# Kernel tuning notes

Hardware: AMD Instinct MI355X
Metric: run time of the kernel (lower is better)

Reference implementation:

```python
import jax, jax.numpy as jnp
import numpy as np
from jax.scipy.special import gammaln, xlogy

B, S, C = 2, 2048, 1536
H, DK, DV = 8, 64, 192
F_REL = C // H  # 192 relative-position features


def positional_features_all(positions, feature_size, seq_length):
    # positions: [1, 2S-1] float32 (signed relative distances)
    n = feature_size // 6  # basis per class per sign
    ap = jnp.abs(positions)  # [1, 2S-1]
    Sf = float(seq_length)
    # exponential decay features
    max_range = float(np.log(Sf) / np.log(2.0))
    half_life = 2.0 ** jnp.linspace(3.0, max_range, n)  # min_half_life = 3.0
    feat_exp = jnp.exp(-jnp.log(2.0) / half_life * ap[..., None])
    # central mask features
    center_widths = 2.0 ** jnp.arange(1, n + 1, dtype=jnp.float32) - 1.0
    feat_cm = (center_widths > ap[..., None]).astype(jnp.float32)
    # gamma pdf features
    stddev = Sf / (2.0 * n)
    start_mean = Sf / n
    mean = jnp.linspace(start_mean, Sf, n)
    conc = (mean / stddev) ** 2
    rate = mean / (stddev ** 2)
    xg = ap[..., None]
    log_unnorm = xlogy(conc - 1.0, xg) - rate * xg
    log_norm = gammaln(conc) - conc * jnp.log(rate)
    prob = jnp.exp(log_unnorm - log_norm) + 1e-8
    feat_g = prob / jnp.max(prob, axis=1, keepdims=True)
    emb = jnp.concatenate([feat_exp, feat_cm, feat_g], axis=-1)  # [1, 2S-1, 3n]
    emb = jnp.concatenate([emb, jnp.sign(positions)[..., None] * emb], axis=-1)
    return emb  # [1, 2S-1, feature_size]


def relative_shift(x):
    # x: [B, H, T, 2T-1] -> [B, H, T, T] (Transformer-XL shift trick)
    b, h, t, _ = x.shape
    x = jnp.pad(x, ((0, 0), (0, 0), (0, 0), (1, 0)))  # [B,H,T,2T]
    x = x.reshape(b, h, 2 * t, t)[:, :, 1:, :]          # [B,H,2T-1,T]
    x = x.reshape(b, h, t, 2 * t - 1)[:, :, :, :t]      # [B,H,T,T]
    return x


def setup_inputs() -> dict:
    key = jax.random.key(0)
    ks = jax.random.split(key, 8)
    inp = {
        "x": jax.random.normal(ks[0], (B, S, C), dtype=jnp.float32),
        "mask": jax.random.randint(ks[1], (B, S), 0, 2, dtype=jnp.int32),
        "Wq": jax.random.normal(ks[2], (C, H * DK), dtype=jnp.float32) * 0.02,
        "Wk": jax.random.normal(ks[3], (C, H * DK), dtype=jnp.float32) * 0.02,
        "Wv": jax.random.normal(ks[4], (C, H * DV), dtype=jnp.float32) * 0.02,
        "Wr": jax.random.normal(ks[5], (F_REL, H * DK), dtype=jnp.float32) * 0.02,
        "r_w_bias": jax.random.normal(ks[6], (1, H, 1, DK), dtype=jnp.float32) * 0.02,
        "Wo": jax.random.normal(ks[7], (H * DV, H * DV), dtype=jnp.float32) * 0.02,
        "bo": jnp.zeros((H * DV,), dtype=jnp.float32),
    }
    return inp


def reference(x, mask, Wq, Wk, Wv, Wr, r_w_bias, Wo, bo):
    b, s, c = x.shape
    # projections -> [B, H, S, d]
    q = (x @ Wq).reshape(b, s, H, DK).transpose(0, 2, 1, 3) * (DK ** -0.5)
    k = (x @ Wk).reshape(b, s, H, DK).transpose(0, 2, 1, 3)
    v = (x @ Wv).reshape(b, s, H, DV).transpose(0, 2, 1, 3)
    # relative positional encodings for distances -S+1 .. S-1
    dist = jnp.arange(-s + 1, s, dtype=jnp.float32)[None, :]  # [1, 2S-1]
    pe = positional_features_all(dist, F_REL, s)               # [1, 2S-1, F_REL]
    r_k = (pe[0] @ Wr).reshape(2 * s - 1, H, DK).transpose(1, 0, 2)  # [H, 2S-1, DK]
    # content + position logits
    content_logits = jnp.einsum('bhqd,bhkd->bhqk', q, k)                   # [B,H,S,S]
    rel_logits = jnp.einsum('bhqd,hkd->bhqk', q + r_w_bias, r_k)           # [B,H,S,2S-1]
    logits = content_logits + relative_shift(rel_logits)
    logits = jnp.where(mask[:, None, None, :] == 0, -1e9, logits)
    weights = jax.nn.softmax(logits, axis=-1)
    out = jnp.einsum('bhqk,bhkd->bhqd', weights, v)  # [B,H,S,DV]
    out = out.transpose(0, 2, 1, 3).reshape(b, s, H * DV)
    return out @ Wo + bo
```

## Files before the change

kernel.cpp:

```cpp
#include <hip/hip_runtime.h>
#include <math.h>

#define SEQ 2048
#define CDIM 1536
#define HN 8
#define DVC 192
#define BN 2
#define NPOS 4095
#define HDK 512
#define HDV 1536
#define PSTR 72

typedef __attribute__((ext_vector_type(8))) _Float16 hf8v;
typedef __attribute__((ext_vector_type(4))) _Float16 hf4v;
typedef __attribute__((ext_vector_type(4))) float f4v;

static __device__ __forceinline__ f4v mfma16(hf8v a, hf8v b, f4v c) {
  return __builtin_amdgcn_mfma_f32_16x16x32_f16(a, b, c, 0, 0, 0);
}
static __device__ __forceinline__ void gl2lds16(const void* g, void* l) {
  __builtin_amdgcn_global_load_lds((const __attribute__((address_space(1))) unsigned int*)g,
                                   (__attribute__((address_space(3))) unsigned int*)l,
                                   16, 0, 0);
}
static __device__ __forceinline__ float rowmax16(float x) {
  x = fmaxf(x, __int_as_float(__builtin_amdgcn_update_dpp(0, __float_as_int(x), 0x128, 0xf, 0xf, true)));
  x = fmaxf(x, __int_as_float(__builtin_amdgcn_update_dpp(0, __float_as_int(x), 0x124, 0xf, 0xf, true)));
  x = fmaxf(x, __int_as_float(__builtin_amdgcn_update_dpp(0, __float_as_int(x), 0x122, 0xf, 0xf, true)));
  x = fmaxf(x, __int_as_float(__builtin_amdgcn_update_dpp(0, __float_as_int(x), 0x121, 0xf, 0xf, true)));
  return x;
}

#define CAST_B 6144
#define TWQ_B  768
#define TWK_B  768
#define TWV_B  2304
#define TWO_B  2304
#define TWR_B  96
#define PREP_BLOCKS (CAST_B + TWQ_B + TWK_B + TWV_B + TWO_B + TWR_B)

__device__ __forceinline__ void twc_tile(const float* __restrict__ W, _Float16* __restrict__ WT,
                                         int K, int N, int tile, float (*tls)[33], int tid) {
  int ntn = N >> 5;
  int nt = tile % ntn, kt = tile / ntn;
  int k0 = kt * 32, n0 = nt * 32;
  int tx = tid & 31, ty = tid >> 5;
#pragma unroll
  for (int p = 0; p < 4; p++) tls[ty + p * 8][tx] = W[(size_t)(k0 + ty + p * 8) * N + n0 + tx];
  __syncthreads();
#pragma unroll
  for (int p = 0; p < 4; p++) {
    int n = ty + p * 8;
    WT[(size_t)(n0 + n) * K + k0 + tx] = (_Float16)tls[tx][n];
  }
}

__global__ __launch_bounds__(256) void prep_kernel(
    const float* __restrict__ x, const float* __restrict__ Wq, const float* __restrict__ Wk,
    const float* __restrict__ Wv, const float* __restrict__ Wo, const float* __restrict__ Wr,
    _Float16* __restrict__ xb, _Float16* __restrict__ WTqkv, _Float16* __restrict__ WoT,
    _Float16* __restrict__ WrT) {
  __shared__ float tls[32][33];
  int blk = blockIdx.x, tid = threadIdx.x;
  if (blk < CAST_B) {
    int i = (blk * 256 + tid) * 4;
    float4 v = *(const float4*)(x + i);
    _Float16 o[4] = {(_Float16)v.x, (_Float16)v.y, (_Float16)v.z, (_Float16)v.w};
    *(unsigned long long*)(xb + i) = *(const unsigned long long*)o;
  } else if (blk < CAST_B + TWQ_B) {
    twc_tile(Wq, WTqkv + 0 * (size_t)CDIM, CDIM, HDK, blk - CAST_B, tls, tid);
  } else if (blk < CAST_B + TWQ_B + TWK_B) {
    twc_tile(Wk, WTqkv + 512 * (size_t)CDIM, CDIM, HDK, blk - (CAST_B + TWQ_B), tls, tid);
  } else if (blk < CAST_B + TWQ_B + TWK_B + TWV_B) {
    twc_tile(Wv, WTqkv + 1024 * (size_t)CDIM, CDIM, HDV, blk - (CAST_B + TWQ_B + TWK_B), tls, tid);
  } else if (blk < CAST_B + TWQ_B + TWK_B + TWV_B + TWO_B) {
    twc_tile(Wo, WoT, CDIM, HDV, blk - (CAST_B + TWQ_B + TWK_B + TWV_B), tls, tid);
  } else {
    twc_tile(Wr, WrT, 192, HDK, blk - (CAST_B + TWQ_B + TWK_B + TWV_B + TWO_B), tls, tid);
  }
}

__global__ __launch_bounds__(256) void pe_kernel(_Float16* __restrict__ pe_h) {
  int idx = blockIdx.x * 256 + threadIdx.x;
  int pos = idx / 96, f = idx - pos * 96;
  float val = 0.0f, sval = 0.0f;
  if (pos < NPOS) {
    float ap = fabsf((float)(pos - (SEQ - 1)));
    int j = f & 31, cls = f >> 5;
    if (cls == 0) {
      float hl = exp2f(3.0f + 8.0f * (float)j / 31.0f);
      val = exp2f(-ap / hl);
    } else if (cls == 1) {
      float cw = exp2f((float)(j + 1)) - 1.0f;
      val = (cw > ap) ? 1.0f : 0.0f;
    } else {
      float conc = 4.0f * (float)((j + 1) * (j + 1));
      float rate = (float)(j + 1) / 16.0f;
      float log_norm = lgammaf(conc) - conc * logf(rate);
      float pv = expf((conc - 1.0f) * logf(ap) - rate * ap - log_norm) + 1e-8f;
      float mode = (conc - 1.0f) / rate;
      float a0 = fminf(floorf(mode), 2047.0f);
      float a1 = fminf(a0 + 1.0f, 2047.0f);
      float p0 = expf((conc - 1.0f) * logf(a0) - rate * a0 - log_norm) + 1e-8f;
      float p1 = expf((conc - 1.0f) * logf(a1) - rate * a1 - log_norm) + 1e-8f;
      val = pv / fmaxf(p0, p1);
    }
    float sgn = (pos > SEQ - 1) ? 1.0f : ((pos < SEQ - 1) ? -1.0f : 0.0f);
    sval = sgn * val;
  }
  pe_h[pos * 192 + f] = (_Float16)val;
  pe_h[pos * 192 + 96 + f] = (_Float16)sval;
}

template <int MODE>
__global__ __launch_bounds__(256, 3) void mfma_gemm(
    const _Float16* __restrict__ A, const _Float16* __restrict__ B,
    const float* __restrict__ bias, void* __restrict__ out0, void* __restrict__ out1,
    void* __restrict__ out2, int K, int ntx) {
  __shared__ __align__(16) _Float16 As[128 * 64];
  __shared__ __align__(16) _Float16 Bs[128 * 64];
  const int tid = threadIdx.x;
  const int lane = tid & 63, l15 = lane & 15, quad = lane >> 4;
  const int wv = tid >> 6;
  const int wm = (wv & 1) * 64, wn = (wv >> 1) * 64;
  const int lin = blockIdx.x;
  const int cpx = gridDim.x >> 3;
  const int sw = (lin & 7) * cpx + (lin >> 3);
  const int row0 = (sw / ntx) * 128, col0 = (sw % ntx) * 128;
  f4v acc[4][4];
#pragma unroll
  for (int i = 0; i < 4; i++)
#pragma unroll
    for (int j = 0; j < 4; j++) acc[i][j] = (f4v)0.0f;

  for (int k0 = 0; k0 < K; k0 += 64) {
    __syncthreads();
#pragma unroll
    for (int p = 0; p < 4; p++) {
      int idx = tid + p * 256;
      int rr = idx >> 3, sc = idx & 7;
      int gc = (sc ^ (rr & 7)) << 3;
      gl2lds16(A + (size_t)(row0 + rr) * K + k0 + gc, As + idx * 8);
      gl2lds16(B + (size_t)(col0 + rr) * K + k0 + gc, Bs + idx * 8);
    }
    __syncthreads();
#pragma unroll
    for (int kc = 0; kc < 2; kc++) {
      hf8v af[4], bfr[4];
#pragma unroll
      for (int t = 0; t < 4; t++) {
        int lrA = wm + t * 16 + l15;
        int lrB = wn + t * 16 + l15;
        af[t]  = *(const hf8v*)(As + lrA * 64 + ((((kc << 2) | quad) ^ (lrA & 7)) << 3));
        bfr[t] = *(const hf8v*)(Bs + lrB * 64 + ((((kc << 2) | quad) ^ (lrB & 7)) << 3));
      }
#pragma unroll
      for (int mt = 0; mt < 4; mt++)
#pragma unroll
        for (int nt = 0; nt < 4; nt++)
          acc[mt][nt] = mfma16(af[mt], bfr[nt], acc[mt][nt]);
    }
  }
#pragma unroll
  for (int mt = 0; mt < 4; mt++)
#pragma unroll
    for (int reg = 0; reg < 4; reg++) {
      int r = row0 + wm + mt * 16 + quad * 4 + reg;
      int bb = r >> 11, ss = r & (SEQ - 1);
#pragma unroll
      for (int nt = 0; nt < 4; nt++) {
        int c = col0 + wn + nt * 16 + l15;
        float vv = acc[mt][nt][reg];
        if (MODE == 0) {
          if (c < 512) {
            ((_Float16*)out0)[(size_t)r * HDK + c] = (_Float16)(vv * 0.125f);
          } else if (c < 1024) {
            int cc = c - 512, h = cc >> 6, d = cc & 63;
            ((_Float16*)out1)[(((size_t)bb * HN + h) * SEQ + ss) * 64 + d] = (_Float16)vv;
          } else {
            int cc = c - 1024, h = cc / DVC, e = cc - h * DVC;
            int jp = (ss & ~63) | ((ss & 15) << 2) | ((ss >> 4) & 3);
            ((_Float16*)out2)[(((size_t)bb * HN + h) * DVC + e) * SEQ + jp] = (_Float16)vv;
          }
        } else if (MODE == 1) {
          int h = c >> 6, d = c & 63;
          ((_Float16*)out0)[((size_t)h * 4096 + r) * 64 + d] = (_Float16)vv;
        } else {
          ((float*)out0)[(size_t)r * HDV + c] = vv + bias[c];
        }
      }
    }
}

template <bool SPLITKV>
__global__ __launch_bounds__(256, 2) void attn_mfma(
    const _Float16* __restrict__ qb, const _Float16* __restrict__ kb,
    const _Float16* __restrict__ vtb, const _Float16* __restrict__ rkb,
    const float* __restrict__ rwb, const int* __restrict__ mask,
    _Float16* __restrict__ attn_out, _Float16* __restrict__ Opart, float* __restrict__ ml) {
  __shared__ __align__(16) _Float16 Vts[192 * 64];
  __shared__ __align__(16) _Float16 RKs[192 * 64];
  __shared__ __align__(16) _Float16 Kts[64 * 64];
  __shared__ __align__(16) _Float16 Pbs[128 * PSTR];

  const int lin = blockIdx.x;
  const int chunk = SPLITKV ? 64 : 32;
  const int swz = (lin & 7) * chunk + (lin >> 3);
  const int bx = swz & 15;
  const int by = swz >> 4;
  const int i0 = bx * 128;
  const int bh = SPLITKV ? (by & 15) : by;
  const int half = SPLITKV ? (by >> 4) : 0;
  const int b = bh >> 3, h = bh & 7;
  const int tid = threadIdx.x;
  const int wv = tid >> 6, lane = tid & 63;
  const int l15 = lane & 15, quad = lane >> 4;

  hf8v qf[2][2], qbf[2][2];
#pragma unroll
  for (int s = 0; s < 2; s++) {
    int qrow = i0 + wv * 32 + s * 16 + l15;
    const _Float16* qp = qb + (size_t)(b * SEQ + qrow) * HDK + h * 64;
#pragma unroll
    for (int kc = 0; kc < 2; kc++) {
      hf8v qv = *(const hf8v*)(qp + kc * 32 + quad * 8);
      qf[s][kc] = qv;
      hf8v t;
#pragma unroll
      for (int j = 0; j < 8; j++)
        t[j] = (_Float16)((float)qv[j] + rwb[h * 64 + kc * 32 + quad * 8 + j]);
      qbf[s][kc] = t;
    }
  }

  f4v Of[2][12];
#pragma unroll
  for (int s = 0; s < 2; s++)
#pragma unroll
    for (int se = 0; se < 12; se++) Of[s][se] = (f4v)0.0f;
  float m_i[2][4] = {{-INFINITY, -INFINITY, -INFINITY, -INFINITY},
                     {-INFINITY, -INFINITY, -INFINITY, -INFINITY}};
  float l_i[2][4] = {{0.f, 0.f, 0.f, 0.f}, {0.f, 0.f, 0.f, 0.f}};

  const int j0beg = SPLITKV ? half * (SEQ / 2) : 0;
  const int j0end = SPLITKV ? j0beg + SEQ / 2 : SEQ;

  for (int j0 = j0beg; j0 < j0end; j0 += 64) {
    __syncthreads();
    int mraw[4];
#pragma unroll
    for (int st = 0; st < 4; st++) mraw[st] = mask[b * SEQ + j0 + st * 16 + l15];
    {
      const int U0 = j0 - i0 + 1920;
#pragma unroll
      for (int r = 0; r < 2; r++) {
        int idx = tid + r * 256, row = idx >> 3, sc = idx & 7;
        gl2lds16(kb + ((size_t)bh * SEQ + j0 + row) * 64 + ((sc ^ (row & 7)) << 3), Kts + idx * 8);
      }
#pragma unroll
      for (int r = 0; r < 6; r++) {
        int idx = tid + r * 256, row = idx >> 3, sc = idx & 7;
        gl2lds16(rkb + ((size_t)h * 4096 + U0 + row) * 64 + ((sc ^ (row & 7)) << 3), RKs + idx * 8);
      }
#pragma unroll
      for (int r = 0; r < 6; r++) {
        int idx = tid + r * 256, row = idx >> 3, sc = idx & 7;
        gl2lds16(vtb + ((size_t)bh * DVC + row) * SEQ + j0 + ((sc ^ (row & 7)) << 3), Vts + idx * 8);
      }
    }
    asm volatile("s_waitcnt vmcnt(6)" ::: "memory");
    __builtin_amdgcn_s_barrier();
    __builtin_amdgcn_sched_barrier(0);
    float mv[4];
#pragma unroll
    for (int st = 0; st < 4; st++) mv[st] = mraw[st] ? 0.f : -1e9f;

#pragma unroll
    for (int s = 0; s < 2; s++) {
      __builtin_amdgcn_s_setprio(1);
      f4v Sf[4];
#pragma unroll
      for (int st = 0; st < 4; st++) {
        Sf[st] = (f4v)0.0f;
#pragma unroll
        for (int kc = 0; kc < 2; kc++) {
          int row = st * 16 + l15;
          hf8v kf = *(const hf8v*)(Kts + row * 64 + ((((kc << 2) | quad) ^ (row & 7)) << 3));
          Sf[st] = mfma16(qf[s][kc], kf, Sf[st]);
        }
      }
      f4v Rf[5];
      const int tb = 112 - 32 * wv - 16 * s;
#pragma unroll
      for (int u = 0; u < 5; u++) {
        Rf[u] = (f4v)0.0f;
#pragma unroll
        for (int kc = 0; kc < 2; kc++) {
          int row = tb + u * 16 + l15;
          hf8v rf = *(const hf8v*)(RKs + row * 64 + ((((kc << 2) | quad) ^ (row & 7)) << 3));
          Rf[u] = mfma16(qbf[s][kc], rf, Rf[u]);
        }
      }
      __builtin_amdgcn_s_setprio(0);
#pragma unroll
      for (int reg = 0; reg < 4; reg++) {
        int delta = l15 - (quad << 2) - reg + 15;
        int srcl = (quad << 4) | (delta & 15);
        float sh0 = __shfl(Rf[0][reg], srcl, 64);
        float sh1 = __shfl(Rf[1][reg], srcl, 64);
        float sh2 = __shfl(Rf[2][reg], srcl, 64);
        float sh3 = __shfl(Rf[3][reg], srcl, 64);
        float sh4 = __shfl(Rf[4][reg], srcl, 64);
        bool hib = delta >= 16;
        Sf[0][reg] += (hib ? sh1 : sh0) + mv[0];
        Sf[1][reg] += (hib ? sh2 : sh1) + mv[1];
        Sf[2][reg] += (hib ? sh3 : sh2) + mv[2];
        Sf[3][reg] += (hib ? sh4 : sh3) + mv[3];
      }
#pragma unroll
      for (int reg = 0; reg < 4; reg++) {
        float t = fmaxf(fmaxf(Sf[0][reg], Sf[1][reg]), fmaxf(Sf[2][reg], Sf[3][reg]));
        t = rowmax16(t);
        if (__any(t - m_i[s][reg] > 8.0f)) {
          float mn = fmaxf(m_i[s][reg], t);
          float alpha = __expf(m_i[s][reg] - mn);
          m_i[s][reg] = mn;
          l_i[s][reg] *= alpha;
#pragma unroll
          for (int se = 0; se < 12; se++) Of[s][se][reg] *= alpha;
        }
        float mcur = m_i[s][reg];
        hf4v pv;
        float rs = 0.f;
#pragma unroll
        for (int st = 0; st < 4; st++) {
          float p = __expf(Sf[st][reg] - mcur);
          rs += p;
          pv[st] = (_Float16)p;
        }
        l_i[s][reg] += rs;
        *(hf4v*)(Pbs + (size_t)(wv * 32 + s * 16 + quad * 4 + reg) * PSTR + l15 * 4) = pv;
      }
    }

    hf8v pa[2][2];
#pragma unroll
    for (int s = 0; s < 2; s++)
#pragma unroll
      for (int kc = 0; kc < 2; kc++)
        pa[s][kc] = *(const hf8v*)(Pbs + (size_t)(wv * 32 + s * 16 + l15) * PSTR +
                                   kc * 32 + quad * 8);
    asm volatile("s_waitcnt vmcnt(0)" ::: "memory");
    __builtin_amdgcn_s_barrier();
    __builtin_amdgcn_sched_barrier(0);
    __builtin_amdgcn_s_setprio(1);
#pragma unroll
    for (int se = 0; se < 12; se++) {
#pragma unroll
      for (int kc = 0; kc < 2; kc++) {
        int row = se * 16 + l15;
        hf8v vf = *(const hf8v*)(Vts + row * 64 + ((((kc << 2) | quad) ^ (row & 7)) << 3));
        Of[0][se] = mfma16(pa[0][kc], vf, Of[0][se]);
        Of[1][se] = mfma16(pa[1][kc], vf, Of[1][se]);
      }
    }
    __builtin_amdgcn_s_setprio(0);
  }

#pragma unroll
  for (int s = 0; s < 2; s++)
#pragma unroll
    for (int reg = 0; reg < 4; reg++) {
      float ls = l_i[s][reg];
      ls += __shfl_xor(ls, 1);
      ls += __shfl_xor(ls, 2);
      ls += __shfl_xor(ls, 4);
      ls += __shfl_xor(ls, 8);
      int row = i0 + wv * 32 + s * 16 + quad * 4 + reg;
      int rg = b * SEQ + row;
      float inv = 1.0f / ls;
      if constexpr (SPLITKV) {
        _Float16* Op = Opart + ((size_t)(half * 4096 + rg)) * HDV + h * DVC;
#pragma unroll
        for (int se = 0; se < 12; se++) Op[se * 16 + l15] = (_Float16)(Of[s][se][reg] * inv);
        if (l15 == 0) {
          size_t mlb = (((size_t)half * 4096 + rg) * HN + h) * 2;
          ml[mlb] = m_i[s][reg];
          ml[mlb + 1] = ls;
        }
      } else {
        size_t base2 = (size_t)rg * HDV + h * DVC;
#pragma unroll
        for (int se = 0; se < 12; se++)
          attn_out[base2 + se * 16 + l15] = (_Float16)(Of[s][se][reg] * inv);
      }
    }
}

__global__ __launch_bounds__(256) void combine_kernel(const _Float16* __restrict__ Opart,
                                                      const float* __restrict__ ml,
                                                      _Float16* __restrict__ attn_out) {
  int i4 = blockIdx.x * 256 + threadIdx.x;
  int rg = i4 / 384, c4 = (i4 - rg * 384) * 4;
  int h = c4 / DVC;
  size_t mlb0 = ((size_t)rg * HN + h) * 2;
  size_t mlb1 = (((size_t)4096 + rg) * HN + h) * 2;
  float m0 = ml[mlb0], l0 = ml[mlb0 + 1];
  float m1 = ml[mlb1], l1 = ml[mlb1 + 1];
  float M = fmaxf(m0, m1);
  float w0 = l0 * __expf(m0 - M), w1 = l1 * __expf(m1 - M);
  float inv = 1.0f / (w0 + w1);
  w0 *= inv;
  w1 *= inv;
  hf4v O0 = *(const hf4v*)(Opart + (size_t)rg * HDV + c4);
  hf4v O1 = *(const hf4v*)(Opart + ((size_t)4096 + rg) * HDV + c4);
  hf4v o;
#pragma unroll
  for (int q = 0; q < 4; q++) o[q] = (_Float16)((float)O0[q] * w0 + (float)O1[q] * w1);
  *(hf4v*)(attn_out + (size_t)rg * HDV + c4) = o;
}

extern "C" void kernel_launch(void* const* d_in, const int* in_sizes, int n_in,
                              void* d_out, int out_size, void* d_ws, size_t ws_size,
                              hipStream_t stream) {
  const float* x    = (const float*)d_in[0];
  const int*   mask = (const int*)d_in[1];
  const float* Wq   = (const float*)d_in[2];
  const float* Wk   = (const float*)d_in[3];
  const float* Wv   = (const float*)d_in[4];
  const float* Wr   = (const float*)d_in[5];
  const float* rwb  = (const float*)d_in[6];
  const float* Wo   = (const float*)d_in[7];
  const float* bo   = (const float*)d_in[8];
  float* out = (float*)d_out;

  char* wsb = (char*)d_ws;
  size_t o = 0;
  auto al = [](size_t v) { return (v + 255) & ~(size_t)255; };
#define CARVE(ptr_t, name, bytes) ptr_t name = (ptr_t)(wsb + o); o = al(o + (bytes));
  CARVE(_Float16*, pe_h, (size_t)4096 * 192 * 2)
  CARVE(_Float16*, WrT, (size_t)HDK * 192 * 2)
  CARVE(_Float16*, xb, (size_t)BN * SEQ * CDIM * 2)
  CARVE(_Float16*, WTqkv, (size_t)2560 * CDIM * 2)
  CARVE(_Float16*, WoT, (size_t)HDV * CDIM * 2)
  CARVE(_Float16*, qb, (size_t)BN * SEQ * HDK * 2)
  CARVE(_Float16*, kb, (size_t)BN * SEQ * HDK * 2)
  CARVE(_Float16*, vtb, (size_t)BN * SEQ * HDV * 2)
  CARVE(_Float16*, rkb, (size_t)HN * 4096 * 64 * 2)
  _Float16* attnh = xb;
  CARVE(_Float16*, Opart, (size_t)2 * 4096 * HDV * 2)
  CARVE(float*, ml, (size_t)2 * 4096 * HN * 2 * 4)
  bool dosplit = (o <= ws_size);

  prep_kernel<<<PREP_BLOCKS, 256, 0, stream>>>(x, Wq, Wk, Wv, Wo, Wr, xb, WTqkv, WoT, WrT);
  pe_kernel<<<4096 * 96 / 256, 256, 0, stream>>>(pe_h);
  mfma_gemm<0><<<640, 256, 0, stream>>>(xb, WTqkv, nullptr, qb, kb, vtb, CDIM, 20);
  mfma_gemm<1><<<128, 256, 0, stream>>>(pe_h, WrT, nullptr, rkb, nullptr, nullptr, 192, 4);
  if (dosplit) {
    attn_mfma<true><<<512, 256, 0, stream>>>(qb, kb, vtb, rkb, rwb, mask,
                                             attnh, Opart, ml);
    combine_kernel<<<4096 * 384 / 256, 256, 0, stream>>>(Opart, ml, attnh);
  } else {
    attn_mfma<false><<<256, 256, 0, stream>>>(qb, kb, vtb, rkb, rwb, mask,
                                              attnh, nullptr, nullptr);
  }
  mfma_gemm<2><<<384, 256, 0, stream>>>(attnh, WoT, bo, out, nullptr, nullptr, CDIM, 12);
}
```

Baseline: 306.7 us.

## Fuse split-KV combine into output projection GEMM with fp32 partials

Removes the separate combine kernel: the attention kernel now writes unnormalized fp32 partial outputs and the output-projection GEMM merges the two KV halves (max/sum rescale) while loading its A tiles. This saves one launch and the fp16 intermediate write/read, but every column tile of the GEMM now re-reads both fp32 partials and recomputes the merge weights, greatly increasing A-side memory traffic. The A loads are also done through registers rather than direct-to-LDS copies.

```diff
diff --git a/kernel.cpp b/kernel.cpp
--- a/kernel.cpp
+++ b/kernel.cpp
@@ -192,12 +192,98 @@
     }
 }
 
+__global__ __launch_bounds__(256, 2) void mfma_gemm_fc(
+    const float* __restrict__ Opart, const float* __restrict__ ml,
+    const _Float16* __restrict__ B, const float* __restrict__ bias,
+    float* __restrict__ out, int ntx) {
+  __shared__ __align__(16) _Float16 As[128 * 64];
+  __shared__ __align__(16) _Float16 Bs[128 * 64];
+  const int K = CDIM;
+  const int tid = threadIdx.x;
+  const int lane = tid & 63, l15 = lane & 15, quad = lane >> 4;
+  const int wv = tid >> 6;
+  const int wm = (wv & 1) * 64, wn = (wv >> 1) * 64;
+  const int lin = blockIdx.x;
+  const int cpx = gridDim.x >> 3;
+  const int sw = (lin & 7) * cpx + (lin >> 3);
+  const int row0 = (sw / ntx) * 128, col0 = (sw % ntx) * 128;
+  f4v acc[4][4];
+#pragma unroll
+  for (int i = 0; i < 4; i++)
+#pragma unroll
+    for (int j = 0; j < 4; j++) acc[i][j] = (f4v)0.0f;
+
+  for (int k0 = 0; k0 < K; k0 += 64) {
+    __syncthreads();
+#pragma unroll
+    for (int p = 0; p < 4; p++) {
+      int idx = tid + p * 256;
+      int rr = idx >> 3, sc = idx & 7;
+      int gc = (sc ^ (rr & 7)) << 3;
+      gl2lds16(B + (size_t)(col0 + rr) * K + k0 + gc, Bs + idx * 8);
+    }
+#pragma unroll
+    for (int p = 0; p < 4; p++) {
+      int idx = tid + p * 256;
+      int rr = idx >> 3, sc = idx & 7;
+      int gc = (sc ^ (rr & 7)) << 3;
+      int rg = row0 + rr;
+      int k = k0 + gc;
+      int h = k / DVC;
+      float2 ml0 = *(const float2*)(ml + (((size_t)rg) * HN + h) * 2);
+      float2 ml1 = *(const float2*)(ml + (((size_t)4096 + rg) * HN + h) * 2);
+      float M = fmaxf(ml0.x, ml1.x);
+      float w0 = __expf(ml0.x - M), w1 = __expf(ml1.x - M);
+      float inv = 1.0f / (ml0.y * w0 + ml1.y * w1);
+      w0 *= inv;
+      w1 *= inv;
+      const float* p0 = Opart + (size_t)rg * HDV + k;
+      const float* p1 = Opart + ((size_t)4096 + rg) * HDV + k;
+      float4 a0 = *(const float4*)(p0), b0 = *(const float4*)(p0 + 4);
+      float4 a1 = *(const float4*)(p1), b1 = *(const float4*)(p1 + 4);
+      _Float16 o[8] = {(_Float16)(a0.x * w0 + a1.x * w1), (_Float16)(a0.y * w0 + a1.y * w1),
+                       (_Float16)(a0.z * w0 + a1.z * w1), (_Float16)(a0.w * w0 + a1.w * w1),
+                       (_Float16)(b0.x * w0 + b1.x * w1), (_Float16)(b0.y * w0 + b1.y * w1),
+                       (_Float16)(b0.z * w0 + b1.z * w1), (_Float16)(b0.w * w0 + b1.w * w1)};
+      *(hf8v*)(As + idx * 8) = *(const hf8v*)o;
+    }
+    __syncthreads();
+#pragma unroll
+    for (int kc = 0; kc < 2; kc++) {
+      hf8v af[4], bfr[4];
+#pragma unroll
+      for (int t = 0; t < 4; t++) {
+        int lrA = wm + t * 16 + l15;
+        int lrB = wn + t * 16 + l15;
+        af[t]  = *(const hf8v*)(As + lrA * 64 + ((((kc << 2) | quad) ^ (lrA & 7)) << 3));
+        bfr[t] = *(const hf8v*)(Bs + lrB * 64 + ((((kc << 2) | quad) ^ (lrB & 7)) << 3));
+      }
+#pragma unroll
+      for (int mt = 0; mt < 4; mt++)
+#pragma unroll
+        for (int nt = 0; nt < 4; nt++)
+          acc[mt][nt] = mfma16(af[mt], bfr[nt], acc[mt][nt]);
+    }
+  }
+#pragma unroll
+  for (int mt = 0; mt < 4; mt++)
+#pragma unroll
+    for (int reg = 0; reg < 4; reg++) {
+      int r = row0 + wm + mt * 16 + quad * 4 + reg;
+#pragma unroll
+      for (int nt = 0; nt < 4; nt++) {
+        int c = col0 + wn + nt * 16 + l15;
+        out[(size_t)r * HDV + c] = acc[mt][nt][reg] + bias[c];
+      }
+    }
+}
+
 template <bool SPLITKV>
 __global__ __launch_bounds__(256, 2) void attn_mfma(
     const _Float16* __restrict__ qb, const _Float16* __restrict__ kb,
     const _Float16* __restrict__ vtb, const _Float16* __restrict__ rkb,
     const float* __restrict__ rwb, const int* __restrict__ mask,
-    _Float16* __restrict__ attn_out, _Float16* __restrict__ Opart, float* __restrict__ ml) {
+    _Float16* __restrict__ attn_out, float* __restrict__ Opart, float* __restrict__ ml) {
   __shared__ __align__(16) _Float16 Vts[192 * 64];
   __shared__ __align__(16) _Float16 RKs[192 * 64];
   __shared__ __align__(16) _Float16 Kts[64 * 64];
@@ -378,46 +464,23 @@
       ls += __shfl_xor(ls, 8);
       int row = i0 + wv * 32 + s * 16 + quad * 4 + reg;
       int rg = b * SEQ + row;
-      float inv = 1.0f / ls;
       if constexpr (SPLITKV) {
-        _Float16* Op = Opart + ((size_t)(half * 4096 + rg)) * HDV + h * DVC;
-#pragma unroll
-        for (int se = 0; se < 12; se++) Op[se * 16 + l15] = (_Float16)(Of[s][se][reg] * inv);
+        float* Op = Opart + ((size_t)(half * 4096 + rg)) * HDV + h * DVC;
+#pragma unroll
+        for (int se = 0; se < 12; se++) Op[se * 16 + l15] = Of[s][se][reg];
         if (l15 == 0) {
           size_t mlb = (((size_t)half * 4096 + rg) * HN + h) * 2;
           ml[mlb] = m_i[s][reg];
           ml[mlb + 1] = ls;
         }
       } else {
+        float inv = 1.0f / ls;
         size_t base2 = (size_t)rg * HDV + h * DVC;
 #pragma unroll
         for (int se = 0; se < 12; se++)
           attn_out[base2 + se * 16 + l15] = (_Float16)(Of[s][se][reg] * inv);
       }
     }
-}
-
-__global__ __launch_bounds__(256) void combine_kernel(const _Float16* __restrict__ Opart,
-                                                      const float* __restrict__ ml,
-                                                      _Float16* __restrict__ attn_out) {
-  int i4 = blockIdx.x * 256 + threadIdx.x;
-  int rg = i4 / 384, c4 = (i4 - rg * 384) * 4;
-  int h = c4 / DVC;
-  size_t mlb0 = ((size_t)rg * HN + h) * 2;
-  size_t mlb1 = (((size_t)4096 + rg) * HN + h) * 2;
-  float m0 = ml[mlb0], l0 = ml[mlb0 + 1];
-  float m1 = ml[mlb1], l1 = ml[mlb1 + 1];
-  float M = fmaxf(m0, m1);
-  float w0 = l0 * __expf(m0 - M), w1 = l1 * __expf(m1 - M);
-  float inv = 1.0f / (w0 + w1);
-  w0 *= inv;
-  w1 *= inv;
-  hf4v O0 = *(const hf4v*)(Opart + (size_t)rg * HDV + c4);
-  hf4v O1 = *(const hf4v*)(Opart + ((size_t)4096 + rg) * HDV + c4);
-  hf4v o;
-#pragma unroll
-  for (int q = 0; q < 4; q++) o[q] = (_Float16)((float)O0[q] * w0 + (float)O1[q] * w1);
-  *(hf4v*)(attn_out + (size_t)rg * HDV + c4) = o;
 }
 
 extern "C" void kernel_launch(void* const* d_in, const int* in_sizes, int n_in,
@@ -448,7 +511,7 @@
   CARVE(_Float16*, vtb, (size_t)BN * SEQ * HDV * 2)
   CARVE(_Float16*, rkb, (size_t)HN * 4096 * 64 * 2)
   _Float16* attnh = xb;
-  CARVE(_Float16*, Opart, (size_t)2 * 4096 * HDV * 2)
+  CARVE(float*, Opart, (size_t)2 * 4096 * HDV * 4)
   CARVE(float*, ml, (size_t)2 * 4096 * HN * 2 * 4)
   bool dosplit = (o <= ws_size);
 
@@ -459,10 +522,10 @@
   if (dosplit) {
     attn_mfma<true><<<512, 256, 0, stream>>>(qb, kb, vtb, rkb, rwb, mask,
                                              attnh, Opart, ml);
-    combine_kernel<<<4096 * 384 / 256, 256, 0, stream>>>(Opart, ml, attnh);
+    mfma_gemm_fc<<<384, 256, 0, stream>>>(Opart, ml, WoT, bo, out, 12);
   } else {
     attn_mfma<false><<<256, 256, 0, stream>>>(qb, kb, vtb, rkb, rwb, mask,
                                               attnh, nullptr, nullptr);
-  }
-  mfma_gemm<2><<<384, 256, 0, stream>>>(attnh, WoT, bo, out, nullptr, nullptr, CDIM, 12);
-}
+    mfma_gemm<2><<<384, 256, 0, stream>>>(attnh, WoT, bo, out, nullptr, nullptr, CDIM, 12);
+  }
+}
```

Measured after the change: 372.7 us. +21.5%, slower.
